# Kernel optimization log

Hardware: AMD Instinct MI355X
Metric: run time of the kernel (lower is better)

Reference implementation:

```python
import jax, jax.numpy as jnp
import numpy as np

DEPTH, HEADS, DIM_HEAD = 3, 8, 64
DIM = 512
MAX_SEQ = 2048
INNER = HEADS * DIM_HEAD  # 512
FF_HID = 4 * DIM          # 2048
EPS = 1e-5


def sparsemax(z):
    # z: (..., n); sparsemax projection onto the simplex (Martins & Astudillo 2016)
    n = z.shape[-1]
    z_sorted = jnp.flip(jnp.sort(z, axis=-1), axis=-1)            # descending
    cs = jnp.cumsum(z_sorted, axis=-1)
    ks = jnp.arange(1, n + 1, dtype=z.dtype)
    support = 1.0 + ks * z_sorted > cs                            # bool
    k_z = jnp.sum(support, axis=-1, keepdims=True)                # int support size
    cs_k = jnp.take_along_axis(cs, k_z - 1, axis=-1)
    tau = (cs_k - 1.0) / k_z.astype(z.dtype)
    return jnp.maximum(z - tau, 0.0)


def layernorm(x, g, b):
    mu = jnp.mean(x, axis=-1, keepdims=True)
    var = jnp.mean(jnp.square(x - mu), axis=-1, keepdims=True)
    return (x - mu) * jax.lax.rsqrt(var + EPS) * g + b


def setup_inputs() -> dict:
    key = jax.random.key(0)
    ks = jax.random.split(key, 12)
    s = 0.02
    inp = {
        "x": jax.random.normal(ks[0], (8, 1024, DIM), dtype=jnp.float32),
        "proj_w": jax.random.normal(ks[1], (DIM, DIM), dtype=jnp.float32) * s,
        "proj_b": jnp.zeros((DIM,), dtype=jnp.float32),
        "pos_emb": jax.random.normal(ks[2], (MAX_SEQ, DIM), dtype=jnp.float32) * s,
        "ln1_g": jnp.ones((DEPTH, DIM), dtype=jnp.float32),
        "ln1_b": jnp.zeros((DEPTH, DIM), dtype=jnp.float32),
        "wqkv": jax.random.normal(ks[3], (DEPTH, DIM, 3 * INNER), dtype=jnp.float32) * s,
        "wout": jax.random.normal(ks[4], (DEPTH, INNER, DIM), dtype=jnp.float32) * s,
        "bout": jnp.zeros((DEPTH, DIM), dtype=jnp.float32),
        "ln2_g": jnp.ones((DEPTH, DIM), dtype=jnp.float32),
        "ln2_b": jnp.zeros((DEPTH, DIM), dtype=jnp.float32),
        "w1": jax.random.normal(ks[5], (DEPTH, DIM, 2 * FF_HID), dtype=jnp.float32) * s,
        "b1": jnp.zeros((DEPTH, 2 * FF_HID), dtype=jnp.float32),
        "w2": jax.random.normal(ks[6], (DEPTH, FF_HID, DIM), dtype=jnp.float32) * s,
        "b2": jnp.zeros((DEPTH, DIM), dtype=jnp.float32),
    }
    return inp


def reference(x, proj_w, proj_b, pos_emb, ln1_g, ln1_b, wqkv, wout, bout,
              ln2_g, ln2_b, w1, b1, w2, b2):
    B, S, D = x.shape
    scale = DIM_HEAD ** -0.5
    x = x @ proj_w + proj_b                       # projection
    x = x + pos_emb[:S][None, :, :]               # positional embedding
    for l in range(DEPTH):
        # --- attention block (Residual(PreNorm(Attention))) ---
        h = layernorm(x, ln1_g[l], ln1_b[l])
        qkv = h @ wqkv[l]                         # (B,S,3*INNER)
        q, k, v = jnp.split(qkv, 3, axis=-1)
        rs = lambda t: t.reshape(B, S, HEADS, DIM_HEAD).transpose(0, 2, 1, 3)
        q, k, v = rs(q), rs(k), rs(v)             # (B,H,S,Dh)
        sim = jnp.einsum('bhid,bhjd->bhij', q, k) * scale
        attn = sparsemax(sim)
        out = jnp.einsum('bhij,bhjd->bhid', attn, v)
        out = out.transpose(0, 2, 1, 3).reshape(B, S, INNER)
        x = x + (out @ wout[l] + bout[l])
        # --- feedforward block (Residual(PreNorm(GEGLU FFN))) ---
        h = layernorm(x, ln2_g[l], ln2_b[l])
        hh = h @ w1[l] + b1[l]                    # (B,S,2*FF_HID)
        a, g = jnp.split(hh, 2, axis=-1)
        ff = (a * jax.nn.gelu(g, approximate=False)) @ w2[l] + b2[l]
        x = x + ff
    return jnp.mean(x, axis=1)                    # (B, D) mean pool
```

## Files before the change

kernel.cpp:

```cpp
#include <hip/hip_runtime.h>
#include <stdint.h>

typedef unsigned short u16;
typedef __attribute__((ext_vector_type(8))) short short8;
typedef __attribute__((ext_vector_type(4))) float f32x4;

__device__ __forceinline__ float bf2f(u16 u){
  union { unsigned u; float f; } v; v.u = ((unsigned)u) << 16; return v.f;
}
__device__ __forceinline__ u16 f2bf(float f){
  union { float f; unsigned u; } v; v.f = f;
  unsigned u = v.u;
  return (u16)((u + 0x7FFFu + ((u >> 16) & 1u)) >> 16);
}
__device__ __forceinline__ void g2lds16(const u16* g, u16* lds){
  __builtin_amdgcn_global_load_lds(
      (const __attribute__((address_space(1))) unsigned int*)g,
      (__attribute__((address_space(3))) unsigned int*)lds, 16, 0, 0);
}
__device__ __forceinline__ float gelu_fast(float g){
  float u2 = g * (1.5957691216057308f + 0.0713548162726f * g * g);
  return g * __builtin_amdgcn_rcpf(1.0f + __expf(-u2));
}

__global__ void k_flag(const unsigned* __restrict__ ln1g, int* __restrict__ flag){
  if (threadIdx.x == 0 && blockIdx.x == 0)
    *flag = (ln1g[0] == 0x3F800000u) ? 0 : 1;
}

__global__ void k_cvt_f32(const void* __restrict__ src, float* __restrict__ dst, int n,
                          const int* __restrict__ flag){
  int i = blockIdx.x * blockDim.x + threadIdx.x;
  if (i < n) dst[i] = (*flag) ? bf2f(((const u16*)src)[i]) : ((const float*)src)[i];
}
__global__ void k_cvt_f32_v8(const void* __restrict__ src, float* __restrict__ dst,
                             const int* __restrict__ flag){
  int i = blockIdx.x * blockDim.x + threadIdx.x;
  if (*flag){
    short8 v = ((const short8*)src)[i];
    float o[8];
    #pragma unroll
    for (int j = 0; j < 8; ++j) o[j] = bf2f((u16)v[j]);
    ((float4*)dst)[i*2]   = *(const float4*)o;
    ((float4*)dst)[i*2+1] = *(const float4*)(o + 4);
  } else {
    ((float4*)dst)[i*2]   = ((const float4*)src)[i*2];
    ((float4*)dst)[i*2+1] = ((const float4*)src)[i*2+1];
  }
}
__global__ void k_cvt_bf16(const void* __restrict__ src, u16* __restrict__ dst, int n,
                           const int* __restrict__ flag){
  int i = blockIdx.x * blockDim.x + threadIdx.x;
  if (i < n) dst[i] = (*flag) ? ((const u16*)src)[i] : f2bf(((const float*)src)[i]);
}
__global__ void k_cvt_bf16_v8(const void* __restrict__ src, u16* __restrict__ dst,
                              const int* __restrict__ flag){
  int i = blockIdx.x * blockDim.x + threadIdx.x;
  if (*flag){
    ((uint4*)dst)[i] = ((const uint4*)src)[i];
  } else {
    float4 a = ((const float4*)src)[i*2];
    float4 b = ((const float4*)src)[i*2+1];
    u16 o[8] = { f2bf(a.x), f2bf(a.y), f2bf(a.z), f2bf(a.w),
                 f2bf(b.x), f2bf(b.y), f2bf(b.z), f2bf(b.w) };
    ((uint4*)dst)[i] = *(const uint4*)o;
  }
}

__global__ void k_transpose(const void* __restrict__ src, u16* __restrict__ dst,
                            int K, int N, const int* __restrict__ flag){
  __shared__ u16 tile[32][33];
  int n0 = blockIdx.x * 32, k0 = blockIdx.y * 32;
  size_t zsrc = (size_t)blockIdx.z * K * N;
  size_t zdst = (size_t)blockIdx.z * N * K;
  int tx = threadIdx.x & 31, ty = threadIdx.x >> 5;
  bool isbf = (*flag) != 0;
  const float* sf = (const float*)src; const u16* sb = (const u16*)src;
  #pragma unroll
  for (int p = 0; p < 4; ++p){
    int kk = k0 + p*8 + ty, nn = n0 + tx;
    size_t idx = zsrc + (size_t)kk * N + nn;
    tile[tx][p*8+ty] = isbf ? sb[idx] : f2bf(sf[idx]);
  }
  __syncthreads();
  #pragma unroll
  for (int p = 0; p < 4; ++p){
    int nn = n0 + p*8 + ty, kk = k0 + tx;
    dst[zdst + (size_t)nn * K + kk] = tile[p*8+ty][tx];
  }
}

__global__ __launch_bounds__(256) void k_ln(const float* __restrict__ x,
                                            const float* __restrict__ g,
                                            const float* __restrict__ b,
                                            u16* __restrict__ out){
  int wv = threadIdx.x >> 6, lane = threadIdx.x & 63;
  int row = blockIdx.x * 4 + wv;
  const float* xr = x + (size_t)row * 512 + lane * 8;
  float4 v0 = *(const float4*)xr;
  float4 v1 = *(const float4*)(xr + 4);
  float s  = v0.x+v0.y+v0.z+v0.w + v1.x+v1.y+v1.z+v1.w;
  float ss = v0.x*v0.x+v0.y*v0.y+v0.z*v0.z+v0.w*v0.w
           + v1.x*v1.x+v1.y*v1.y+v1.z*v1.z+v1.w*v1.w;
  #pragma unroll
  for (int off = 1; off < 64; off <<= 1){ s += __shfl_xor(s, off, 64); ss += __shfl_xor(ss, off, 64); }
  float mu = s * (1.f/512.f);
  float var = ss * (1.f/512.f) - mu*mu;
  float rs = rsqrtf(var + 1e-5f);
  const float* gp = g + lane*8; const float* bp = b + lane*8;
  float4 g0 = *(const float4*)gp, g1 = *(const float4*)(gp+4);
  float4 b0 = *(const float4*)bp, b1 = *(const float4*)(bp+4);
  u16 o[8];
  o[0]=f2bf((v0.x-mu)*rs*g0.x+b0.x); o[1]=f2bf((v0.y-mu)*rs*g0.y+b0.y);
  o[2]=f2bf((v0.z-mu)*rs*g0.z+b0.z); o[3]=f2bf((v0.w-mu)*rs*g0.w+b0.w);
  o[4]=f2bf((v1.x-mu)*rs*g1.x+b1.x); o[5]=f2bf((v1.y-mu)*rs*g1.y+b1.y);
  o[6]=f2bf((v1.z-mu)*rs*g1.z+b1.z); o[7]=f2bf((v1.w-mu)*rs*g1.w+b1.w);
  *(uint4*)(out + (size_t)row*512 + lane*8) = *(const uint4*)o;
}

__global__ __launch_bounds__(256) void k_gemm(const u16* __restrict__ A,
                                              const u16* __restrict__ Wt, int K, int mode,
                                              float* __restrict__ xres, u16* __restrict__ out16,
                                              const float* __restrict__ bias,
                                              const float* __restrict__ pos){
  __shared__ u16 As[128*64];
  __shared__ u16 Bs[128*64];
  const int tid = threadIdx.x;
  const int wv = tid >> 6, lane = tid & 63;
  const int lm = lane & 15, lq = lane >> 4;
  const int wm = (wv >> 1) * 64, wn = (wv & 1) * 64;
  const int m0 = blockIdx.y * 128, n0 = blockIdx.x * 128;
  const int lrow = lane >> 3;
  const int scol = ((lane & 7) ^ lrow) << 3;
  f32x4 acc[4][4];
  #pragma unroll
  for (int i = 0; i < 4; ++i)
    #pragma unroll
    for (int j = 0; j < 4; ++j){ f32x4 z = {0.f,0.f,0.f,0.f}; acc[i][j] = z; }

  for (int k0 = 0; k0 < K; k0 += 64){
    #pragma unroll
    for (int it = 0; it < 4; ++it){
      int ci = wv*4 + it;
      int row = ci*8 + lrow;
      g2lds16(&A [(size_t)(m0 + row) * K + k0 + scol], &As[ci*512]);
      g2lds16(&Wt[(size_t)(n0 + row) * K + k0 + scol], &Bs[ci*512]);
    }
    __syncthreads();
    #pragma unroll
    for (int kk = 0; kk < 2; ++kk){
      short8 af[4], bf[4];
      #pragma unroll
      for (int t = 0; t < 4; ++t){
        int cs = ((kk*4 + lq) ^ (lm & 7)) << 3;
        af[t] = *(const short8*)&As[(wm + t*16 + lm)*64 + cs];
        bf[t] = *(const short8*)&Bs[(wn + t*16 + lm)*64 + cs];
      }
      #pragma unroll
      for (int i = 0; i < 4; ++i)
        #pragma unroll
        for (int j = 0; j < 4; ++j)
          acc[i][j] = __builtin_amdgcn_mfma_f32_16x16x32_bf16(af[i], bf[j], acc[i][j], 0, 0, 0);
    }
    __syncthreads();
  }
  #pragma unroll
  for (int i = 0; i < 4; ++i)
    #pragma unroll
    for (int j = 0; j < 4; ++j)
      #pragma unroll
      for (int r = 0; r < 4; ++r){
        int row = m0 + wm + i*16 + lq*4 + r;
        int col = n0 + wn + j*16 + lm;
        float v = acc[i][j][r];
        if (mode == 0){
          xres[(size_t)row*512 + col] = v + bias[col] + pos[(size_t)(row & 1023)*512 + col];
        } else if (mode == 1){
          int part = col >> 9, within = col & 511;
          int head = within >> 6, dh = within & 63;
          int b = row >> 10, s = row & 1023;
          int bh = b*8 + head;
          size_t o;
          if (part < 2) o = (size_t)part*4194304 + (((size_t)bh*1024 + s) << 6) + dh;
          else          o = (size_t)8388608 + (size_t)bh*65536 + (size_t)dh*1024 + s;
          out16[o] = f2bf(v);
        } else {
          size_t idx = (size_t)row*512 + col;
          xres[idx] = xres[idx] + v + bias[col];
        }
      }
}

__global__ __launch_bounds__(256) void k_gemm64(const u16* __restrict__ A,
                                                const u16* __restrict__ Wt, int K, int mode,
                                                float* __restrict__ xres,
                                                const float* __restrict__ bias,
                                                const float* __restrict__ pos){
  __shared__ u16 As[64*64];
  __shared__ u16 Bs[128*64];
  const int tid = threadIdx.x;
  const int wv = tid >> 6, lane = tid & 63;
  const int lm = lane & 15, lq = lane >> 4;
  const int wm = (wv >> 1) * 32, wn = (wv & 1) * 64;
  const int m0 = blockIdx.y * 64, n0 = blockIdx.x * 128;
  const int lrow = lane >> 3;
  const int scol = ((lane & 7) ^ lrow) << 3;
  f32x4 acc[2][4];
  #pragma unroll
  for (int i = 0; i < 2; ++i)
    #pragma unroll
    for (int j = 0; j < 4; ++j){ f32x4 z = {0.f,0.f,0.f,0.f}; acc[i][j] = z; }

  for (int k0 = 0; k0 < K; k0 += 64){
    #pragma unroll
    for (int it = 0; it < 2; ++it){
      int ci = wv*2 + it;
      int row = ci*8 + lrow;
      g2lds16(&A[(size_t)(m0 + row) * K + k0 + scol], &As[ci*512]);
    }
    #pragma unroll
    for (int it = 0; it < 4; ++it){
      int ci = wv*4 + it;
      int row = ci*8 + lrow;
      g2lds16(&Wt[(size_t)(n0 + row) * K + k0 + scol], &Bs[ci*512]);
    }
    __syncthreads();
    #pragma unroll
    for (int kk = 0; kk < 2; ++kk){
      short8 af[2], bf[4];
      int cs = ((kk*4 + lq) ^ (lm & 7)) << 3;
      #pragma unroll
      for (int t = 0; t < 2; ++t)
        af[t] = *(const short8*)&As[(wm + t*16 + lm)*64 + cs];
      #pragma unroll
      for (int t = 0; t < 4; ++t)
        bf[t] = *(const short8*)&Bs[(wn + t*16 + lm)*64 + cs];
      #pragma unroll
      for (int i = 0; i < 2; ++i)
        #pragma unroll
        for (int j = 0; j < 4; ++j)
          acc[i][j] = __builtin_amdgcn_mfma_f32_16x16x32_bf16(af[i], bf[j], acc[i][j], 0, 0, 0);
    }
    __syncthreads();
  }
  #pragma unroll
  for (int i = 0; i < 2; ++i)
    #pragma unroll
    for (int j = 0; j < 4; ++j)
      #pragma unroll
      for (int r = 0; r < 4; ++r){
        int row = m0 + wm + i*16 + lq*4 + r;
        int col = n0 + wn + j*16 + lm;
        float v = acc[i][j][r];
        if (mode == 0){
          xres[(size_t)row*512 + col] = v + bias[col] + pos[(size_t)(row & 1023)*512 + col];
        } else {
          size_t idx = (size_t)row*512 + col;
          xres[idx] = xres[idx] + v + bias[col];
        }
      }
}

__global__ __launch_bounds__(256) void k_ff1_geglu64(const u16* __restrict__ A,
                                                     const u16* __restrict__ W1t,
                                                     const float* __restrict__ b1,
                                                     u16* __restrict__ ffh){
  __shared__ u16 As[64*64];
  __shared__ u16 Ba[128*64];
  __shared__ u16 Bg[128*64];
  const int tid = threadIdx.x;
  const int wv = tid >> 6, lane = tid & 63;
  const int lm = lane & 15, lq = lane >> 4;
  const int wm = (wv >> 1) * 32, wn = (wv & 1) * 64;
  const int m0 = blockIdx.y * 64, n0 = blockIdx.x * 128;
  const int lrow = lane >> 3;
  const int scol = ((lane & 7) ^ lrow) << 3;
  const int K = 512;
  f32x4 aa[2][4], ag[2][4];
  #pragma unroll
  for (int i = 0; i < 2; ++i)
    #pragma unroll
    for (int j = 0; j < 4; ++j){ f32x4 z = {0.f,0.f,0.f,0.f}; aa[i][j] = z; ag[i][j] = z; }
  for (int k0 = 0; k0 < K; k0 += 64){
    #pragma unroll
    for (int it = 0; it < 2; ++it){
      int ci = wv*2 + it;
      int row = ci*8 + lrow;
      g2lds16(&A[(size_t)(m0 + row) * K + k0 + scol], &As[ci*512]);
    }
    #pragma unroll
    for (int it = 0; it < 4; ++it){
      int ci = wv*4 + it;
      int row = ci*8 + lrow;
      g2lds16(&W1t[(size_t)(n0 + row) * K + k0 + scol],        &Ba[ci*512]);
      g2lds16(&W1t[(size_t)(2048 + n0 + row) * K + k0 + scol], &Bg[ci*512]);
    }
    __syncthreads();
    #pragma unroll
    for (int kk = 0; kk < 2; ++kk){
      short8 af[2], ba[4], bg[4];
      int cs = ((kk*4 + lq) ^ (lm & 7)) << 3;
      #pragma unroll
      for (int t = 0; t < 2; ++t)
        af[t] = *(const short8*)&As[(wm + t*16 + lm)*64 + cs];
      #pragma unroll
      for (int t = 0; t < 4; ++t){
        ba[t] = *(const short8*)&Ba[(wn + t*16 + lm)*64 + cs];
        bg[t] = *(const short8*)&Bg[(wn + t*16 + lm)*64 + cs];
      }
      #pragma unroll
      for (int i = 0; i < 2; ++i)
        #pragma unroll
        for (int j = 0; j < 4; ++j){
          aa[i][j] = __builtin_amdgcn_mfma_f32_16x16x32_bf16(af[i], ba[j], aa[i][j], 0, 0, 0);
          ag[i][j] = __builtin_amdgcn_mfma_f32_16x16x32_bf16(af[i], bg[j], ag[i][j], 0, 0, 0);
        }
    }
    __syncthreads();
  }
  #pragma unroll
  for (int i = 0; i < 2; ++i)
    #pragma unroll
    for (int j = 0; j < 4; ++j)
      #pragma unroll
      for (int r = 0; r < 4; ++r){
        int row = m0 + wm + i*16 + lq*4 + r;
        int n = n0 + wn + j*16 + lm;
        float a = aa[i][j][r] + b1[n];
        float g = ag[i][j][r] + b1[2048 + n];
        ffh[(size_t)row*2048 + n] = f2bf(a * gelu_fast(g));
      }
}

__global__ __launch_bounds__(1024) void k_attn2(const u16* __restrict__ qb,
                                                const u16* __restrict__ kb,
                                                const u16* __restrict__ vt,
                                                u16* __restrict__ aout){
  __shared__ u16 Sm[16*1024];
  __shared__ float Pp[4*16*64];
  const int tid = threadIdx.x;
  const int wv = tid >> 6, lane = tid & 63;
  const int lm = lane & 15, lq = lane >> 4;
  int fid = blockIdx.x;
  int nf = (fid & 7) * 512 + (fid >> 3);
  const int bh = nf >> 6;
  const int q0 = (nf & 63) * 16;
  const size_t base = (size_t)bh * 65536;
  const u16* qp = &qb[base + (size_t)(q0 + lm)*64 + lq*8];
  short8 qf0 = *(const short8*)qp;
  short8 qf1 = *(const short8*)(qp + 32);
  {
    const int kt = wv;
    #pragma unroll
    for (int j = 0; j < 4; ++j){
      const u16* kp = &kb[base + (size_t)(kt*64 + j*16 + lm)*64 + lq*8];
      short8 kf0 = *(const short8*)kp;
      short8 kf1 = *(const short8*)(kp + 32);
      f32x4 a = {0.f,0.f,0.f,0.f};
      a = __builtin_amdgcn_mfma_f32_16x16x32_bf16(qf0, kf0, a, 0, 0, 0);
      a = __builtin_amdgcn_mfma_f32_16x16x32_bf16(qf1, kf1, a, 0, 0, 0);
      int col = kt*64 + j*16 + lm;
      int cc = col >> 3, c7 = col & 7;
      #pragma unroll
      for (int r = 0; r < 4; ++r){
        int row = lq*4 + r;
        Sm[row*1024 + ((cc ^ (row & 7)) << 3) + c7] = f2bf(a[r] * 0.125f);
      }
    }
  }
  __syncthreads();
  {
    const int row = wv, r7 = row & 7;
    u16* lo = &Sm[row*1024 + ((lane ^ r7) << 3)];
    u16* hi = &Sm[row*1024 + (((64 + lane) ^ r7) << 3)];
    u16 zb[16];
    *(uint4*)zb       = *(const uint4*)lo;
    *(uint4*)(zb + 8) = *(const uint4*)hi;
    float z[16];
    #pragma unroll
    for (int i = 0; i < 16; ++i) z[i] = bf2f(zb[i]);
    float s0 = 0.f;
    #pragma unroll
    for (int i = 0; i < 16; ++i) s0 += z[i];
    #pragma unroll
    for (int off = 1; off < 64; off <<= 1) s0 += __shfl_xor(s0, off, 64);
    float tau = (s0 - 1.0f) * (1.0f/1024.0f);
    int prevc = 1024;
    #pragma unroll 1
    for (int it = 0; it < 32; ++it){
      float sz = 0.f; int c = 0;
      #pragma unroll
      for (int i = 0; i < 16; ++i){
        bool aq = z[i] > tau;
        sz += aq ? z[i] : 0.f;
        c  += (int)__popcll(__ballot(aq));
      }
      #pragma unroll
      for (int off = 1; off < 64; off <<= 1) sz += __shfl_xor(sz, off, 64);
      tau = (sz - 1.0f) * __builtin_amdgcn_rcpf((float)c);
      if (c >= prevc) break;
      prevc = c;
    }
    u16 pb[16];
    #pragma unroll
    for (int i = 0; i < 16; ++i){
      float p = z[i] - tau;
      pb[i] = f2bf(p > 0.f ? p : 0.f);
    }
    *(uint4*)lo = *(const uint4*)pb;
    *(uint4*)(hi) = *(const uint4*)(pb + 8);
  }
  __syncthreads();
  {
    const int ds = wv & 3, kc = wv >> 2;
    f32x4 acc = {0.f,0.f,0.f,0.f};
    const u16* vrow = &vt[base + (size_t)(ds*16 + lm)*1024 + lq*8];
    #pragma unroll
    for (int k0 = kc*256; k0 < kc*256 + 256; k0 += 32){
      int cc = (k0 >> 3) + lq;
      short8 pa = *(const short8*)&Sm[lm*1024 + ((cc ^ (lm & 7)) << 3)];
      short8 vb = *(const short8*)(vrow + k0);
      acc = __builtin_amdgcn_mfma_f32_16x16x32_bf16(pa, vb, acc, 0, 0, 0);
    }
    #pragma unroll
    for (int r = 0; r < 4; ++r)
      Pp[(kc*16 + lq*4 + r)*64 + ds*16 + lm] = acc[r];
  }
  __syncthreads();
  {
    int s = tid >> 6, d = tid & 63;
    int o = s*64 + d;
    float v = Pp[o] + Pp[1024 + o] + Pp[2048 + o] + Pp[3072 + o];
    int b = bh >> 3, h = bh & 7;
    aout[((size_t)(b*1024 + q0 + s))*512 + h*64 + d] = f2bf(v);
  }
}

__global__ __launch_bounds__(256) void k_pool1(const float* __restrict__ xres,
                                               float* __restrict__ part){
  int b = blockIdx.y, ch = blockIdx.x, tid = threadIdx.x;
  float a0 = 0.f, a1 = 0.f;
  for (int i = 0; i < 64; ++i){
    const float* r = xres + ((size_t)(b*1024 + ch*64 + i)) * 512;
    a0 += r[tid]; a1 += r[tid + 256];
  }
  part[((size_t)(b*16 + ch))*512 + tid]       = a0;
  part[((size_t)(b*16 + ch))*512 + tid + 256] = a1;
}
__global__ __launch_bounds__(512) void k_pool2(const float* __restrict__ part,
                                               void* __restrict__ out,
                                               const int* __restrict__ flag){
  int b = blockIdx.x, d = threadIdx.x;
  float s = 0.f;
  for (int c = 0; c < 16; ++c) s += part[((size_t)(b*16 + c))*512 + d];
  s *= (1.0f/1024.0f);
  if (*flag) ((u16*)out)[b*512 + d] = f2bf(s);
  else       ((float*)out)[b*512 + d] = s;
}

extern "C" void kernel_launch(void* const* d_in, const int* in_sizes, int n_in,
                              void* d_out, int out_size, void* d_ws, size_t ws_size,
                              hipStream_t stream){
  (void)in_sizes; (void)n_in; (void)out_size; (void)ws_size;
  char* w = (char*)d_ws;
  size_t off = 0;
  auto alloc = [&](size_t bytes) -> char* {
    char* p = w + off;
    off += (bytes + 255) & ~(size_t)255;
    return p;
  };
  int*   flag  = (int*)  alloc(4);
  float* xres  = (float*)alloc((size_t)8192*512*4);
  u16*   hb    = (u16*)  alloc((size_t)8192*512*2);
  u16*   qb    = (u16*)  alloc((size_t)8388608);
  u16*   kb    = (u16*)  alloc((size_t)8388608);
  u16*   vtb   = (u16*)  alloc((size_t)8388608);
  u16*   aoutb = (u16*)  alloc((size_t)8388608);
  u16*   ffh   = qb;
  u16*   pwT   = (u16*)  alloc((size_t)512*512*2);
  u16*   wqkvT = (u16*)  alloc((size_t)3*1536*512*2);
  u16*   woutT = (u16*)  alloc((size_t)3*512*512*2);
  u16*   w1T   = (u16*)  alloc((size_t)3*4096*512*2);
  u16*   w2T   = (u16*)  alloc((size_t)3*512*2048*2);
  float* posf  = (float*)alloc((size_t)1024*512*4);
  float* pbf   = (float*)alloc(512*4);
  float* ln1gf = (float*)alloc(1536*4);
  float* ln1bf = (float*)alloc(1536*4);
  float* ln2gf = (float*)alloc(1536*4);
  float* ln2bf = (float*)alloc(1536*4);
  float* boutf = (float*)alloc(1536*4);
  float* b1f   = (float*)alloc(12288*4);
  float* b2f   = (float*)alloc(1536*4);
  float* part  = (float*)alloc((size_t)8*16*512*4);

  const void* x_raw = d_in[0];  const void* projw = d_in[1];  const void* projb = d_in[2];
  const void* pose  = d_in[3];  const void* ln1g  = d_in[4];  const void* ln1b  = d_in[5];
  const void* wqkv  = d_in[6];  const void* wout  = d_in[7];  const void* bout  = d_in[8];
  const void* ln2g  = d_in[9];  const void* ln2b  = d_in[10]; const void* w1    = d_in[11];
  const void* b1    = d_in[12]; const void* w2    = d_in[13]; const void* b2    = d_in[14];

  k_flag<<<1, 1, 0, stream>>>((const unsigned*)ln1g, flag);

  k_transpose<<<dim3(16, 16, 1), 256, 0, stream>>>(projw, pwT,   512,  512, flag);
  k_transpose<<<dim3(48, 16, 3), 256, 0, stream>>>(wqkv,  wqkvT, 512, 1536, flag);
  k_transpose<<<dim3(16, 16, 3), 256, 0, stream>>>(wout,  woutT, 512,  512, flag);
  k_transpose<<<dim3(128,16, 3), 256, 0, stream>>>(w1,    w1T,   512, 4096, flag);
  k_transpose<<<dim3(16, 64, 3), 256, 0, stream>>>(w2,    w2T,  2048,  512, flag);

  k_cvt_f32<<<2,    256, 0, stream>>>(projb, pbf,    512,    flag);
  k_cvt_f32_v8<<<256, 256, 0, stream>>>(pose, posf, flag);
  k_cvt_f32<<<6,    256, 0, stream>>>(ln1g,  ln1gf,  1536,   flag);
  k_cvt_f32<<<6,    256, 0, stream>>>(ln1b,  ln1bf,  1536,   flag);
  k_cvt_f32<<<6,    256, 0, stream>>>(ln2g,  ln2gf,  1536,   flag);
  k_cvt_f32<<<6,    256, 0, stream>>>(ln2b,  ln2bf,  1536,   flag);
  k_cvt_f32<<<6,    256, 0, stream>>>(bout,  boutf,  1536,   flag);
  k_cvt_f32<<<48,   256, 0, stream>>>(b1,    b1f,    12288,  flag);
  k_cvt_f32<<<6,    256, 0, stream>>>(b2,    b2f,    1536,   flag);
  k_cvt_bf16_v8<<<2048, 256, 0, stream>>>(x_raw, hb, flag);

  k_gemm64<<<dim3(4, 128), 256, 0, stream>>>(hb, pwT, 512, 0, xres, pbf, posf);

  for (int l = 0; l < 3; ++l){
    k_ln<<<2048, 256, 0, stream>>>(xres, ln1gf + l*512, ln1bf + l*512, hb);
    k_gemm<<<dim3(12, 64), 256, 0, stream>>>(hb, wqkvT + (size_t)l*1536*512, 512, 1,
                                             nullptr, qb, nullptr, nullptr);
    k_attn2<<<dim3(4096), 1024, 0, stream>>>(qb, kb, vtb, aoutb);
    k_gemm64<<<dim3(4, 128), 256, 0, stream>>>(aoutb, woutT + (size_t)l*512*512, 512, 2,
                                               xres, boutf + l*512, nullptr);
    k_ln<<<2048, 256, 0, stream>>>(xres, ln2gf + l*512, ln2bf + l*512, hb);
    k_ff1_geglu64<<<dim3(16, 128), 256, 0, stream>>>(hb, w1T + (size_t)l*4096*512,
                                                     b1f + l*4096, ffh);
    k_gemm64<<<dim3(4, 128), 256, 0, stream>>>(ffh, w2T + (size_t)l*512*2048, 2048, 2,
                                               xres, b2f + l*512, nullptr);
  }
  k_pool1<<<dim3(16, 8), 256, 0, stream>>>(xres, part);
  k_pool2<<<8, 512, 0, stream>>>(part, d_out, flag);
}
```

Measured before the change: 1.100 ms.

## Use safeguarded Newton-bisection for sparsemax tau with DPP wave reductions

Replaces the monotone Michelot-style fixed-point iteration for the sparsemax threshold with a bracketed Newton/bisection search seeded by the row mean and max, stopping when the simplex residual is small. Wave-wide sums now use DPP row operations plus two shuffles, and the count is reduced as a float alongside the sum instead of through ballot/popcount. The aim is fewer iterations and cheaper reductions per iteration. In exchange the loop body does more scalar work, and the residual tolerance changes when iteration stops, which may slightly alter the threshold.

Result: slower. 1.165 ms (+5.9%).

```diff
diff --git a/kernel.cpp b/kernel.cpp
--- a/kernel.cpp
+++ b/kernel.cpp
@@ -21,6 +21,27 @@
 __device__ __forceinline__ float gelu_fast(float g){
   float u2 = g * (1.5957691216057308f + 0.0713548162726f * g * g);
   return g * __builtin_amdgcn_rcpf(1.0f + __expf(-u2));
+}
+
+template<int C>
+__device__ __forceinline__ float dppf(float x){
+  return __int_as_float(__builtin_amdgcn_update_dpp(0, __float_as_int(x), C, 0xF, 0xF, true));
+}
+__device__ __forceinline__ void wsum2(float& a, float& b){
+  a += dppf<0xB1>(a);  b += dppf<0xB1>(b);
+  a += dppf<0x4E>(a);  b += dppf<0x4E>(b);
+  a += dppf<0x124>(a); b += dppf<0x124>(b);
+  a += dppf<0x128>(a); b += dppf<0x128>(b);
+  a += __shfl_xor(a, 16, 64); b += __shfl_xor(b, 16, 64);
+  a += __shfl_xor(a, 32, 64); b += __shfl_xor(b, 32, 64);
+}
+__device__ __forceinline__ void wsummax(float& s, float& m){
+  s += dppf<0xB1>(s);  m = fmaxf(m, dppf<0xB1>(m));
+  s += dppf<0x4E>(s);  m = fmaxf(m, dppf<0x4E>(m));
+  s += dppf<0x124>(s); m = fmaxf(m, dppf<0x124>(m));
+  s += dppf<0x128>(s); m = fmaxf(m, dppf<0x128>(m));
+  s += __shfl_xor(s, 16, 64); m = fmaxf(m, __shfl_xor(m, 16, 64));
+  s += __shfl_xor(s, 32, 64); m = fmaxf(m, __shfl_xor(m, 32, 64));
 }
 
 __global__ void k_flag(const unsigned* __restrict__ ln1g, int* __restrict__ flag){
@@ -371,35 +392,42 @@
   __syncthreads();
   {
     const int row = wv, r7 = row & 7;
-    u16* lo = &Sm[row*1024 + ((lane ^ r7) << 3)];
-    u16* hi = &Sm[row*1024 + (((64 + lane) ^ r7) << 3)];
+    u16* plo = &Sm[row*1024 + ((lane ^ r7) << 3)];
+    u16* phi = &Sm[row*1024 + (((64 + lane) ^ r7) << 3)];
     u16 zb[16];
-    *(uint4*)zb       = *(const uint4*)lo;
-    *(uint4*)(zb + 8) = *(const uint4*)hi;
+    *(uint4*)zb       = *(const uint4*)plo;
+    *(uint4*)(zb + 8) = *(const uint4*)phi;
     float z[16];
     #pragma unroll
     for (int i = 0; i < 16; ++i) z[i] = bf2f(zb[i]);
-    float s0 = 0.f;
-    #pragma unroll
-    for (int i = 0; i < 16; ++i) s0 += z[i];
-    #pragma unroll
-    for (int off = 1; off < 64; off <<= 1) s0 += __shfl_xor(s0, off, 64);
-    float tau = (s0 - 1.0f) * (1.0f/1024.0f);
-    int prevc = 1024;
+    float s0 = z[0], mx = z[0];
+    #pragma unroll
+    for (int i = 1; i < 16; ++i){ s0 += z[i]; mx = fmaxf(mx, z[i]); }
+    wsummax(s0, mx);
+    float lo = (s0 - 1.0f) * (1.0f/1024.0f);
+    float hi = mx;
+    float tau = lo;
     #pragma unroll 1
-    for (int it = 0; it < 32; ++it){
-      float sz = 0.f; int c = 0;
+    for (int it = 0; it < 24; ++it){
+      float sz = 0.f, cn = 0.f;
       #pragma unroll
       for (int i = 0; i < 16; ++i){
-        bool aq = z[i] > tau;
-        sz += aq ? z[i] : 0.f;
-        c  += (int)__popcll(__ballot(aq));
-      }
-      #pragma unroll
-      for (int off = 1; off < 64; off <<= 1) sz += __shfl_xor(sz, off, 64);
-      tau = (sz - 1.0f) * __builtin_amdgcn_rcpf((float)c);
-      if (c >= prevc) break;
-      prevc = c;
+        bool a = z[i] > tau;
+        sz += a ? z[i] : 0.f;
+        cn += a ? 1.f : 0.f;
+      }
+      wsum2(sz, cn);
+      float f  = sz - cn * tau - 1.0f;
+      float tN = (sz - 1.0f) * __builtin_amdgcn_rcpf(cn);
+      if (fabsf(f) < 1e-5f) break;
+      if (f > 0.f) lo = tau; else hi = tau;
+      float mid = 0.5f * (lo + hi);
+      bool inb = (tN > lo) && (tN < hi);
+      float tnew;
+      if (f > 0.f) tnew = fmaxf(inb ? tN : lo, mid);
+      else         tnew = inb ? tN : mid;
+      if (tnew == tau) break;
+      tau = tnew;
     }
     u16 pb[16];
     #pragma unroll
@@ -407,8 +435,8 @@
       float p = z[i] - tau;
       pb[i] = f2bf(p > 0.f ? p : 0.f);
     }
-    *(uint4*)lo = *(const uint4*)pb;
-    *(uint4*)(hi) = *(const uint4*)(pb + 8);
+    *(uint4*)plo = *(const uint4*)pb;
+    *(uint4*)phi = *(const uint4*)(pb + 8);
   }
   __syncthreads();
   {
```
